# Performance work log

Measured on AMD Instinct MI355X. Metric: run time of the kernel, lower is better.

## Reference

```python
import jax, jax.numpy as jnp
import numpy as np

D = 1024
N_HEAD = 16
D_HEAD = D // N_HEAD
B, S = 4, 2048
EPS = 1e-6


def rmsnorm(x, w):
    # x: [..., d_head]
    return x / jnp.sqrt(jnp.mean(x * x, axis=-1, keepdims=True) + EPS) * w


def setup_inputs() -> dict:
    key = jax.random.key(0)
    ks = jax.random.split(key, 6)
    x = jax.random.normal(ks[0], (B, S, D), dtype=jnp.float32)
    # causal mask: True means masked (upper triangle above diagonal)
    mask = jnp.triu(jnp.ones((S, S), dtype=bool), k=1)
    scale = 1.0 / np.sqrt(D)
    W_qkv = jax.random.normal(ks[1], (D, 3 * D), dtype=jnp.float32) * scale
    b_qkv = jnp.zeros((3 * D,), dtype=jnp.float32)
    W_o = jax.random.normal(ks[2], (D, D), dtype=jnp.float32) * scale
    b_o = jnp.zeros((D,), dtype=jnp.float32)
    wq = jnp.ones((D_HEAD,), dtype=jnp.float32)
    wk = jnp.ones((D_HEAD,), dtype=jnp.float32)
    return {"x": x, "mask": mask, "W_qkv": W_qkv, "b_qkv": b_qkv,
            "W_o": W_o, "b_o": b_o, "wq": wq, "wk": wk}


def reference(x, mask, W_qkv, b_qkv, W_o, b_o, wq, wk):
    b, s, d = x.shape
    qkv = x @ W_qkv + b_qkv  # [b,s,3d]
    q, k, v = jnp.split(qkv, 3, axis=-1)
    q = q.reshape(b, s, N_HEAD, D_HEAD)
    k = k.reshape(b, s, N_HEAD, D_HEAD)
    v = v.reshape(b, s, N_HEAD, D_HEAD)
    q = rmsnorm(q, wq)
    k = rmsnorm(k, wk)
    # NOTE: no 1/sqrt(d_head) scaling, faithful to the source
    attn = jnp.einsum('bqhd,bkhd->bhqk', q, k)
    attn = jnp.where(mask[None, None, :, :], -jnp.inf, attn)
    attn = jax.nn.softmax(attn, axis=-1)
    z = jnp.einsum('bhqk,bkhd->bqhd', attn, v).reshape(b, s, d)
    return z @ W_o + b_o
```

## Files before the change

kernel.cpp:

```cpp
#include <hip/hip_runtime.h>
#include <cmath>

typedef _Float16 half_t;
typedef _Float16 half8 __attribute__((ext_vector_type(8)));
typedef _Float16 half4v __attribute__((ext_vector_type(4)));
typedef float float4v __attribute__((ext_vector_type(4)));

#define LOG2E 1.44269504088896340736f

#define GLDS16(g, l)                                                                   \
    __builtin_amdgcn_global_load_lds((const __attribute__((address_space(1))) void*)(g), \
                                     (__attribute__((address_space(3))) void*)(l), 16, 0, 0)

__global__ void cast_f32_f16(const float* __restrict__ in, half_t* __restrict__ out, int n) {
    int i = (blockIdx.x * blockDim.x + threadIdx.x) * 4;
    if (i >= n) return;
    float4 v = *(const float4*)(in + i);
    half4v o;
    o[0] = (half_t)v.x; o[1] = (half_t)v.y; o[2] = (half_t)v.z; o[3] = (half_t)v.w;
    *(half4v*)(out + i) = o;
}

__global__ void transpose_cast(const float* __restrict__ in, half_t* __restrict__ out, int R, int C) {
    __shared__ float tile[32][33];
    int c0 = blockIdx.x * 32, r0 = blockIdx.y * 32;
    int tx = threadIdx.x, ty = threadIdx.y;
    for (int p = 0; p < 4; p++) {
        int r = r0 + ty + p * 8;
        tile[ty + p * 8][tx] = in[(size_t)r * C + c0 + tx];
    }
    __syncthreads();
    for (int p = 0; p < 4; p++) {
        int c = c0 + ty + p * 8;
        out[(size_t)c * R + r0 + tx] = (half_t)tile[tx][ty + p * 8];
    }
}

template <int OUT_F16>
__global__ __launch_bounds__(256) void gemm_f16(
    const half_t* __restrict__ A,
    const half_t* __restrict__ Bt,
    const float* __restrict__ bias,
    void* __restrict__ Cout,
    int M, int N, int K)
{
    __shared__ __align__(16) half_t As[128 * 32];
    __shared__ __align__(16) half_t Bs[128 * 32];
    int t = threadIdx.x;
    int lane = t & 63, w = t >> 6;
    int m0 = blockIdx.x * 128, n0 = blockIdx.y * 128;
    int wm = (w >> 1) * 64, wn = (w & 1) * 64;
    int lrow = lane & 15, quad = lane >> 4;

    int srow = t >> 2, scol = (t & 3) * 8;
    const half_t* gA = A  + (size_t)(m0 + srow) * K + scol;
    const half_t* gB = Bt + (size_t)(n0 + srow) * K + scol;
    half_t* ldsA = As + w * 512;
    half_t* ldsB = Bs + w * 512;

    float4v acc[4][4] = {};

    for (int k0 = 0; k0 < K; k0 += 32) {
        __syncthreads();
        GLDS16(gA + k0,               ldsA);
        GLDS16(gA + (size_t)64 * K + k0, ldsA + 2048);
        GLDS16(gB + k0,               ldsB);
        GLDS16(gB + (size_t)64 * K + k0, ldsB + 2048);
        __asm__ volatile("s_waitcnt vmcnt(0)" ::: "memory");
        __syncthreads();
        half8 af[4], bf[4];
        for (int i = 0; i < 4; i++) af[i] = *(const half8*)(&As[(wm + i * 16 + lrow) * 32 + quad * 8]);
        for (int i = 0; i < 4; i++) bf[i] = *(const half8*)(&Bs[(wn + i * 16 + lrow) * 32 + quad * 8]);
        for (int mi = 0; mi < 4; mi++)
            for (int ni = 0; ni < 4; ni++)
                acc[mi][ni] = __builtin_amdgcn_mfma_f32_16x16x32_f16(af[mi], bf[ni], acc[mi][ni], 0, 0, 0);
    }

    for (int mi = 0; mi < 4; mi++)
        for (int ni = 0; ni < 4; ni++)
            for (int r = 0; r < 4; r++) {
                int gr = m0 + wm + mi * 16 + quad * 4 + r;
                int gc = n0 + wn + ni * 16 + lrow;
                float v = acc[mi][ni][r] + bias[gc];
                if (OUT_F16) ((half_t*)Cout)[(size_t)gr * N + gc] = (half_t)v;
                else         ((float*)Cout)[(size_t)gr * N + gc] = v;
            }
}

__global__ void rmsnorm_qk(const half_t* __restrict__ qkv,
                           const float* __restrict__ wq, const float* __restrict__ wk,
                           half_t* __restrict__ Qh, half_t* __restrict__ Kh) {
    int row = blockIdx.x;
    int b = row >> 11, s = row & 2047;
    int t = threadIdx.x;
    int isK = t >> 6;
    int tt = t & 63;
    int head = tt >> 2, chunk = tt & 3;
    const half_t* src = qkv + (size_t)row * 3072 + isK * 1024 + head * 64 + chunk * 16;
    half8 h0 = *(const half8*)(src);
    half8 h1 = *(const half8*)(src + 8);
    float v[16];
    for (int i = 0; i < 8; i++) { v[i] = (float)h0[i]; v[8 + i] = (float)h1[i]; }
    float ss = 0.f;
    for (int i = 0; i < 16; i++) ss += v[i] * v[i];
    ss += __shfl_xor(ss, 1);
    ss += __shfl_xor(ss, 2);
    float rr = rsqrtf(ss * (1.0f / 64.0f) + 1e-6f);
    const float* wv = (isK ? wk : wq) + chunk * 16;
    half_t* dst = (isK ? Kh : Qh) + ((size_t)((b * 16 + head) * 2048 + s)) * 64 + chunk * 16;
    half8 o0, o1;
    for (int i = 0; i < 8; i++) {
        o0[i] = (half_t)(v[i] * rr * wv[i]);
        o1[i] = (half_t)(v[8 + i] * rr * wv[8 + i]);
    }
    *(half8*)(dst) = o0;
    *(half8*)(dst + 8) = o1;
}

__global__ void v_transpose(const half_t* __restrict__ qkv, half_t* __restrict__ Vt) {
    __shared__ half_t tile[32][40];
    int s0 = blockIdx.x * 32;
    int d0 = blockIdx.y * 32;
    int bh = blockIdx.z;
    int b = bh >> 4, h = bh & 15;
    int tx = threadIdx.x, ty = threadIdx.y;
    for (int p = 0; p < 4; p++) {
        int s = s0 + ty + p * 8;
        tile[ty + p * 8][tx] = qkv[((size_t)(b * 2048 + s)) * 3072 + 2048 + h * 64 + d0 + tx];
    }
    __syncthreads();
    for (int p = 0; p < 4; p++) {
        int d = d0 + ty + p * 8;
        Vt[((size_t)bh * 64 + d) * 2048 + s0 + tx] = tile[tx][ty + p * 8];
    }
}

__global__ __launch_bounds__(256, 4) void attn(
    const half_t* __restrict__ Qh, const half_t* __restrict__ Kh, const half_t* __restrict__ Vt,
    half_t* __restrict__ Z)
{
    __shared__ __align__(16) half_t Ks[64][88];
    __shared__ __align__(16) half_t Vs[64][88];
    __shared__ __align__(16) half_t Ps[4][16][88];

    int bh = blockIdx.y;
    int b = bh >> 4, h = bh & 15;
    int t = threadIdx.x, lane = t & 63, w = t >> 6;
    int lrow = lane & 15, quad = lane >> 4;

    for (int pass = 0; pass < 2; pass++) {
        int qt = pass ? (31 - (int)blockIdx.x) : (int)blockIdx.x;
        int qb = qt * 64;
        int q0w = qb + w * 16;

        const half_t* Qbase = Qh + ((size_t)bh * 2048 + q0w + lrow) * 64;
        half8 qf0 = *(const half8*)(Qbase + quad * 8);
        half8 qf1 = *(const half8*)(Qbase + 32 + quad * 8);

        float4v ot[4] = {};
        float m = -__builtin_inff(), l = 0.f;

        for (int kt = 0; kt <= qt; kt++) {
            int kb = kt * 64;
            __syncthreads();
            for (int j = 0; j < 2; j++) {
                int r = (t >> 3) + 32 * j, c = (t & 7) * 8;
                *(uint4*)(&Ks[r][c]) = *(const uint4*)(Kh + ((size_t)bh * 2048 + kb + r) * 64 + c);
                *(uint4*)(&Vs[r][c]) = *(const uint4*)(Vt + ((size_t)bh * 64 + r) * 2048 + kb + c);
            }
            __syncthreads();

            float4v st[4];
            for (int f = 0; f < 4; f++) {
                float4v z = {};
                half8 k0 = *(const half8*)(&Ks[f * 16 + lrow][quad * 8]);
                half8 k1 = *(const half8*)(&Ks[f * 16 + lrow][32 + quad * 8]);
                z = __builtin_amdgcn_mfma_f32_16x16x32_f16(k0, qf0, z, 0, 0, 0);
                z = __builtin_amdgcn_mfma_f32_16x16x32_f16(k1, qf1, z, 0, 0, 0);
                st[f] = z;
            }
            if (kt == qt) {
                int qrel = w * 16 + lrow;
                for (int f = 0; f < 4; f++)
                    for (int r = 0; r < 4; r++) {
                        int krel = f * 16 + quad * 4 + r;
                        if (krel > qrel) st[f][r] = -__builtin_inff();
                    }
            }
            float tm = st[0][0];
            for (int f = 0; f < 4; f++)
                for (int r = 0; r < 4; r++) tm = fmaxf(tm, st[f][r]);
            tm = fmaxf(tm, __shfl_xor(tm, 16));
            tm = fmaxf(tm, __shfl_xor(tm, 32));
            float mn = fmaxf(m, tm);
            float alpha = exp2f((m - mn) * LOG2E);
            m = mn;
            float rs = 0.f;
            for (int f = 0; f < 4; f++) {
                half4v ph;
                for (int r = 0; r < 4; r++) {
                    float p = exp2f((st[f][r] - mn) * LOG2E);
                    rs += p;
                    ph[r] = (half_t)p;
                }
                *(half4v*)(&Ps[w][lrow][f * 16 + quad * 4]) = ph;
            }
            rs += __shfl_xor(rs, 16);
            rs += __shfl_xor(rs, 32);
            l = l * alpha + rs;
            for (int f2 = 0; f2 < 4; f2++)
                for (int r = 0; r < 4; r++) ot[f2][r] *= alpha;

            __asm__ volatile("s_waitcnt lgkmcnt(0)" ::: "memory");
            half8 p0 = *(const half8*)(&Ps[w][lrow][quad * 8]);
            half8 p1 = *(const half8*)(&Ps[w][lrow][32 + quad * 8]);
            for (int f2 = 0; f2 < 4; f2++) {
                half8 v0 = *(const half8*)(&Vs[f2 * 16 + lrow][quad * 8]);
                half8 v1 = *(const half8*)(&Vs[f2 * 16 + lrow][32 + quad * 8]);
                ot[f2] = __builtin_amdgcn_mfma_f32_16x16x32_f16(v0, p0, ot[f2], 0, 0, 0);
                ot[f2] = __builtin_amdgcn_mfma_f32_16x16x32_f16(v1, p1, ot[f2], 0, 0, 0);
            }
        }

        float inv = 1.0f / l;
        size_t base = ((size_t)(b * 2048) + q0w + lrow) * 1024 + h * 64;
        for (int f2 = 0; f2 < 4; f2++) {
            half4v oh;
            for (int r = 0; r < 4; r++) oh[r] = (half_t)(ot[f2][r] * inv);
            *(half4v*)(Z + base + f2 * 16 + quad * 4) = oh;
        }
    }
}

extern "C" void kernel_launch(void* const* d_in, const int* in_sizes, int n_in,
                              void* d_out, int out_size, void* d_ws, size_t ws_size,
                              hipStream_t stream)
{
    const float* x     = (const float*)d_in[0];
    const float* W_qkv = (const float*)d_in[2];
    const float* b_qkv = (const float*)d_in[3];
    const float* W_o   = (const float*)d_in[4];
    const float* b_o   = (const float*)d_in[5];
    const float* wq    = (const float*)d_in[6];
    const float* wk    = (const float*)d_in[7];
    float* out = (float*)d_out;

    char* ws = (char*)d_ws;
    half_t* xh  = (half_t*)(ws);
    half_t* Wqt = (half_t*)(ws + (16ull << 20));
    half_t* Wot = (half_t*)(ws + (22ull << 20));
    half_t* qkv = (half_t*)(ws + (24ull << 20));
    half_t* Qh  = (half_t*)(ws + (72ull << 20));
    half_t* Kh  = (half_t*)(ws + (88ull << 20));
    half_t* Vt  = (half_t*)(ws + (104ull << 20));
    half_t* zh  = xh;

    cast_f32_f16<<<8192, 256, 0, stream>>>(x, xh, 8192 * 1024);
    transpose_cast<<<dim3(96, 32), dim3(32, 8), 0, stream>>>(W_qkv, Wqt, 1024, 3072);
    transpose_cast<<<dim3(32, 32), dim3(32, 8), 0, stream>>>(W_o, Wot, 1024, 1024);
    gemm_f16<1><<<dim3(64, 24), 256, 0, stream>>>(xh, Wqt, b_qkv, qkv, 8192, 3072, 1024);
    rmsnorm_qk<<<8192, 128, 0, stream>>>(qkv, wq, wk, Qh, Kh);
    v_transpose<<<dim3(64, 2, 64), dim3(32, 8), 0, stream>>>(qkv, Vt);
    attn<<<dim3(16, 64), 256, 0, stream>>>(Qh, Kh, Vt, zh);
    gemm_f16<0><<<dim3(64, 8), 256, 0, stream>>>(zh, Wot, b_o, out, 8192, 1024, 1024);
}
```

Measured before the change: 322.7 us.

## Enlarge attention query tile to 128 rows with async XOR-swizzled LDS loads

The attention kernel now runs 8 waves per block, each handling 16 query rows, so a block covers 128 queries and each loaded K/V tile is reused by twice as many waves. K/V tiles are loaded with direct global-to-LDS loads into an XOR-swizzled, unpadded layout in place of register-staged padded copies. The P buffer uses the same swizzle. Waves whose rows lie entirely before a key tile skip compute but still join the loads and barriers, so causal imbalance inside a block grows and occupancy may drop with the larger block.

```diff
diff --git a/kernel.cpp b/kernel.cpp
--- a/kernel.cpp
+++ b/kernel.cpp
@@ -62,9 +62,9 @@
 
     for (int k0 = 0; k0 < K; k0 += 32) {
         __syncthreads();
-        GLDS16(gA + k0,               ldsA);
+        GLDS16(gA + k0,                  ldsA);
         GLDS16(gA + (size_t)64 * K + k0, ldsA + 2048);
-        GLDS16(gB + k0,               ldsB);
+        GLDS16(gB + k0,                  ldsB);
         GLDS16(gB + (size_t)64 * K + k0, ldsB + 2048);
         __asm__ volatile("s_waitcnt vmcnt(0)" ::: "memory");
         __syncthreads();
@@ -135,22 +135,34 @@
     }
 }
 
-__global__ __launch_bounds__(256, 4) void attn(
+__global__ __launch_bounds__(512, 4) void attn(
     const half_t* __restrict__ Qh, const half_t* __restrict__ Kh, const half_t* __restrict__ Vt,
     half_t* __restrict__ Z)
 {
-    __shared__ __align__(16) half_t Ks[64][88];
-    __shared__ __align__(16) half_t Vs[64][88];
-    __shared__ __align__(16) half_t Ps[4][16][88];
+    __shared__ __align__(16) half_t Ks[64 * 64];
+    __shared__ __align__(16) half_t Vs[64 * 64];
+    __shared__ __align__(16) half_t Ps[8 * 16 * 64];
 
     int bh = blockIdx.y;
     int b = bh >> 4, h = bh & 15;
     int t = threadIdx.x, lane = t & 63, w = t >> 6;
     int lrow = lane & 15, quad = lane >> 4;
 
+    int sr = w * 8 + (lane >> 3);
+    int sc = (lane & 7) ^ ((lane >> 3) & 7);
+    const half_t* gK0 = Kh + ((size_t)bh * 2048 + sr) * 64 + sc * 8;
+    const half_t* gV0 = Vt + ((size_t)bh * 64 + sr) * 2048 + sc * 8;
+    half_t* ldsK = Ks + w * 512;
+    half_t* ldsV = Vs + w * 512;
+
+    int sw = lrow & 7;
+    int cA = (quad ^ sw) * 8;
+    int cB = ((quad + 4) ^ sw) * 8;
+    half_t* PsW = Ps + w * 1024 + lrow * 64;
+
     for (int pass = 0; pass < 2; pass++) {
-        int qt = pass ? (31 - (int)blockIdx.x) : (int)blockIdx.x;
-        int qb = qt * 64;
+        int qt = pass ? (15 - (int)blockIdx.x) : (int)blockIdx.x;
+        int qb = qt * 128;
         int q0w = qb + w * 16;
 
         const half_t* Qbase = Qh + ((size_t)bh * 2048 + q0w + lrow) * 64;
@@ -160,31 +172,32 @@
         float4v ot[4] = {};
         float m = -__builtin_inff(), l = 0.f;
 
-        for (int kt = 0; kt <= qt; kt++) {
+        int nt = 2 * qt + 2;
+        for (int kt = 0; kt < nt; kt++) {
             int kb = kt * 64;
             __syncthreads();
-            for (int j = 0; j < 2; j++) {
-                int r = (t >> 3) + 32 * j, c = (t & 7) * 8;
-                *(uint4*)(&Ks[r][c]) = *(const uint4*)(Kh + ((size_t)bh * 2048 + kb + r) * 64 + c);
-                *(uint4*)(&Vs[r][c]) = *(const uint4*)(Vt + ((size_t)bh * 64 + r) * 2048 + kb + c);
-            }
+            GLDS16(gK0 + (size_t)kb * 64, ldsK);
+            GLDS16(gV0 + kb,              ldsV);
+            __asm__ volatile("s_waitcnt vmcnt(0)" ::: "memory");
             __syncthreads();
+            if (kb > q0w + 15) continue;
 
             float4v st[4];
             for (int f = 0; f < 4; f++) {
                 float4v z = {};
-                half8 k0 = *(const half8*)(&Ks[f * 16 + lrow][quad * 8]);
-                half8 k1 = *(const half8*)(&Ks[f * 16 + lrow][32 + quad * 8]);
+                const half_t* kr = Ks + (f * 16 + lrow) * 64;
+                half8 k0 = *(const half8*)(kr + cA);
+                half8 k1 = *(const half8*)(kr + cB);
                 z = __builtin_amdgcn_mfma_f32_16x16x32_f16(k0, qf0, z, 0, 0, 0);
                 z = __builtin_amdgcn_mfma_f32_16x16x32_f16(k1, qf1, z, 0, 0, 0);
                 st[f] = z;
             }
-            if (kt == qt) {
-                int qrel = w * 16 + lrow;
+            if (kb + 63 > q0w) {
+                int qabs = q0w + lrow;
                 for (int f = 0; f < 4; f++)
                     for (int r = 0; r < 4; r++) {
-                        int krel = f * 16 + quad * 4 + r;
-                        if (krel > qrel) st[f][r] = -__builtin_inff();
+                        int key = kb + f * 16 + quad * 4 + r;
+                        if (key > qabs) st[f][r] = -__builtin_inff();
                     }
             }
             float tm = st[0][0];
@@ -203,7 +216,8 @@
                     rs += p;
                     ph[r] = (half_t)p;
                 }
-                *(half4v*)(&Ps[w][lrow][f * 16 + quad * 4]) = ph;
+                int cc = (2 * f + (quad >> 1)) ^ sw;
+                *(half4v*)(PsW + cc * 8 + (quad & 1) * 4) = ph;
             }
             rs += __shfl_xor(rs, 16);
             rs += __shfl_xor(rs, 32);
@@ -212,11 +226,12 @@
                 for (int r = 0; r < 4; r++) ot[f2][r] *= alpha;
 
             __asm__ volatile("s_waitcnt lgkmcnt(0)" ::: "memory");
-            half8 p0 = *(const half8*)(&Ps[w][lrow][quad * 8]);
-            half8 p1 = *(const half8*)(&Ps[w][lrow][32 + quad * 8]);
+            half8 p0 = *(const half8*)(PsW + cA);
+            half8 p1 = *(const half8*)(PsW + cB);
             for (int f2 = 0; f2 < 4; f2++) {
-                half8 v0 = *(const half8*)(&Vs[f2 * 16 + lrow][quad * 8]);
-                half8 v1 = *(const half8*)(&Vs[f2 * 16 + lrow][32 + quad * 8]);
+                const half_t* vr = Vs + (f2 * 16 + lrow) * 64;
+                half8 v0 = *(const half8*)(vr + cA);
+                half8 v1 = *(const half8*)(vr + cB);
                 ot[f2] = __builtin_amdgcn_mfma_f32_16x16x32_f16(v0, p0, ot[f2], 0, 0, 0);
                 ot[f2] = __builtin_amdgcn_mfma_f32_16x16x32_f16(v1, p1, ot[f2], 0, 0, 0);
             }
@@ -261,6 +276,6 @@
     gemm_f16<1><<<dim3(64, 24), 256, 0, stream>>>(xh, Wqt, b_qkv, qkv, 8192, 3072, 1024);
     rmsnorm_qk<<<8192, 128, 0, stream>>>(qkv, wq, wk, Qh, Kh);
     v_transpose<<<dim3(64, 2, 64), dim3(32, 8), 0, stream>>>(qkv, Vt);
-    attn<<<dim3(16, 64), 256, 0, stream>>>(Qh, Kh, Vt, zh);
+    attn<<<dim3(8, 64), 512, 0, stream>>>(Qh, Kh, Vt, zh);
     gemm_f16<0><<<dim3(64, 8), 256, 0, stream>>>(zh, Wot, b_o, out, 8192, 1024, 1024);
 }
```

Result: slower. 330.7 us (+2.5%).
